# Optimization experiments

Hardware: AMD Instinct MI355X
Metric: run time of the kernel (lower is better)

## Reference

```python
import jax, jax.numpy as jnp
import numpy as np

EMB = 64
D = 2 * EMB          # 128, feature dim of R / hidden of attention MLP
B, L = 128, 4096     # batch, sequence length
N_ITER = 50          # bisection iterations (entmax_bisect default)


def entmax_bisect(X, alpha, n_iter=N_ITER):
    """alpha-entmax via bisection over the last axis. X: [B, L], alpha: [B, 1] (>1)."""
    am1 = alpha - 1.0
    Xs = X * am1
    d = X.shape[-1]
    inv = 1.0 / am1
    max_val = jnp.max(Xs, axis=-1, keepdims=True)
    tau_lo0 = max_val - 1.0                       # gp(1, alpha) = 1
    tau_hi = max_val - (1.0 / d) ** am1           # gp(1/d, alpha)

    def p(tau):
        return jnp.clip(Xs - tau, 0.0, None) ** inv

    f_lo = jnp.sum(p(tau_lo0), axis=-1, keepdims=True) - 1.0

    def body(i, carry):
        tau_lo, dm, _ = carry
        dm = dm * 0.5
        tau_m = tau_lo + dm
        f_m = jnp.sum(p(tau_m), axis=-1, keepdims=True) - 1.0
        tau_lo = jnp.where(f_m * f_lo >= 0, tau_m, tau_lo)
        return (tau_lo, dm, tau_m)

    _, _, tau_m = jax.lax.fori_loop(0, n_iter, body, (tau_lo0, tau_hi - tau_lo0, tau_lo0))
    p_m = p(tau_m)
    return p_m / jnp.sum(p_m, axis=-1, keepdims=True)  # ensure_sum_one


def setup_inputs() -> dict:
    key = jax.random.key(0)
    ks = jax.random.split(key, 9)
    s = 1.0 / np.sqrt(D)
    R = jax.random.normal(ks[0], (B, L, D), dtype=jnp.float32)
    alpha = 1.25 + 0.5 * jax.random.uniform(ks[1], (B, 1), dtype=jnp.float32)  # in (1.25, 1.75)
    target = jax.random.normal(ks[2], (B, 1, D), dtype=jnp.float32)
    Wr1 = s * jax.random.normal(ks[3], (D, D), dtype=jnp.float32)      # Linear(2E, 2E), no bias
    Wr2 = s * jax.random.normal(ks[4], (D, EMB), dtype=jnp.float32)    # Linear(E, 2E) (shape-fixed), no bias
    Wr3 = s * jax.random.normal(ks[5], (1, D), dtype=jnp.float32)      # Linear(2E, 1), no bias
    bias_r = s * jax.random.normal(ks[6], (D,), dtype=jnp.float32)
    Wf_w = s * jax.random.normal(ks[7], (EMB, D), dtype=jnp.float32)   # Linear(2E, E)
    Wf_b = s * jax.random.normal(ks[8], (EMB,), dtype=jnp.float32)
    return {"R": R, "alpha": alpha, "target": target, "Wr1": Wr1, "Wr2": Wr2,
            "Wr3": Wr3, "bias_r": bias_r, "Wf_w": Wf_w, "Wf_b": Wf_b}


def reference(R, alpha, target, Wr1, Wr2, Wr3, bias_r, Wf_w, Wf_b):
    # q = Wf(target): [B, 1, E]
    q = jnp.einsum('btd,ed->bte', target, Wf_w) + Wf_b
    # additive attention score: Wr3 @ relu(Wr1 k + Wr2 q + b): [B, L]
    h = jax.nn.relu(jnp.einsum('bld,ed->ble', R, Wr1)
                    + jnp.einsum('bte,de->btd', q, Wr2)
                    + bias_r)
    scores = jnp.einsum('bld,d->bl', h, Wr3[0])
    # entmax sparsification over the sequence axis
    a = entmax_bisect(scores, alpha)
    # weighted sum of v = R: [B, D]
    res = jnp.einsum('bl,bld->bd', a, R)
    res = jax.nn.selu(res)
    res = res / jnp.linalg.norm(res, axis=-1, keepdims=True)
    return res
```

## Files before the change

kernel.cpp:

```cpp
#include <hip/hip_runtime.h>
#include <hip/hip_bf16.h>

#define B_ 128
#define L_ 4096
#define D_ 128
#define E_ 64

typedef __attribute__((ext_vector_type(8))) short short8;
typedef __attribute__((ext_vector_type(4))) float floatx4;

static __device__ __forceinline__ void split_trunc(float x, unsigned short& hs,
                                                   unsigned short& ls) {
  unsigned int bx = __float_as_uint(x);
  float hf = __uint_as_float(bx & 0xffff0000u);
  hs = (unsigned short)(bx >> 16);
  float lo = x - hf;
  ls = (unsigned short)(__float_as_uint(lo) >> 16);
}

__global__ __launch_bounds__(256) void prep(
    const float* __restrict__ Wr1, unsigned short* __restrict__ hi,
    unsigned short* __restrict__ lo, const float* __restrict__ target,
    const float* __restrict__ Wr2, const float* __restrict__ bias_r,
    const float* __restrict__ Wf_w, const float* __restrict__ Wf_b,
    float* __restrict__ cvec) {
  if (blockIdx.x < 64) {
    int t = blockIdx.x * 256 + threadIdx.x;
    int j = t & 7, lane = (t >> 3) & 63, ks = (t >> 9) & 3, nt = t >> 11;
    int e = nt * 16 + (lane & 15);
    int d = ks * 32 + (lane >> 4) * 8 + j;
    split_trunc(Wr1[e * D_ + d], hi[t], lo[t]);
  } else {
    const int sub = threadIdx.x >> 7;
    const int t = threadIdx.x & 127;
    const int b = (blockIdx.x - 64) * 2 + sub;
    __shared__ float tg[2][D_];
    __shared__ float q[2][E_];
    tg[sub][t] = target[b * D_ + t];
    __syncthreads();
    if (t < E_) {
      float s = Wf_b[t];
      #pragma unroll 8
      for (int d = 0; d < D_; ++d) s += tg[sub][d] * Wf_w[t * D_ + d];
      q[sub][t] = s;
    }
    __syncthreads();
    float s = bias_r[t];
    #pragma unroll 8
    for (int e = 0; e < E_; ++e) s += q[sub][e] * Wr2[t * E_ + e];
    cvec[b * D_ + t] = s;
  }
}

__global__ __launch_bounds__(256, 4) void pass_b(
    const float* __restrict__ R, const unsigned short* __restrict__ Whi,
    const unsigned short* __restrict__ Wlo, const float* __restrict__ cvec,
    const float* __restrict__ Wr3, float* __restrict__ scores) {
  __shared__ __align__(16) unsigned short sAhi[8192];
  __shared__ __align__(16) unsigned short sAlo[8192];
  __shared__ float red[256];

  const int b = blockIdx.x >> 6;
  const int lt = blockIdx.x & 63;
  const int t = threadIdx.x;
  const int wave = t >> 6, lane = t & 63;
  const int col = lane & 15, quad = lane >> 4;

  float w3[2], cb[2];
  #pragma unroll
  for (int n = 0; n < 2; ++n) {
    const int e = (wave * 2 + n) * 16 + col;
    w3[n] = Wr3[e];
    cb[n] = cvec[b * D_ + e];
  }

  const float* Rbase = R + ((size_t)b * L_ + (size_t)lt * 64) * D_;
  #pragma unroll
  for (int ks = 0; ks < 4; ++ks) {
    const int row = wave * 16 + col;
    const int c0 = ks * 32 + quad * 8;
    const float4* p = (const float4*)(Rbase + (size_t)row * D_ + c0);
    float4 v0 = p[0], v1 = p[1];
    float vv[8] = {v0.x, v0.y, v0.z, v0.w, v1.x, v1.y, v1.z, v1.w};
    union { unsigned short u[8]; short8 v; } H, Lo;
    #pragma unroll
    for (int j = 0; j < 8; ++j) split_trunc(vv[j], H.u[j], Lo.u[j]);
    const int base = ((wave * 4 + ks) * 64 + lane) * 8;
    *(short8*)(sAhi + base) = H.v;
    *(short8*)(sAlo + base) = Lo.v;
  }

  short8 bh[2][4], bl[2][4];
  #pragma unroll
  for (int n = 0; n < 2; ++n)
    #pragma unroll
    for (int ks = 0; ks < 4; ++ks) {
      const int off = (((wave * 2 + n) * 4 + ks) * 64 + lane) * 8;
      bh[n][ks] = *(const short8*)(Whi + off);
      bl[n][ks] = *(const short8*)(Wlo + off);
    }

  floatx4 acc[4][2];
  #pragma unroll
  for (int mt = 0; mt < 4; ++mt)
    #pragma unroll
    for (int n = 0; n < 2; ++n) acc[mt][n] = (floatx4){0.f, 0.f, 0.f, 0.f};

  __syncthreads();

  #pragma unroll
  for (int mt = 0; mt < 4; ++mt) {
    #pragma unroll
    for (int ks = 0; ks < 4; ++ks) {
      const int ai = ((mt * 4 + ks) * 64 + lane) * 8;
      short8 ah = *(const short8*)(sAhi + ai);
      short8 al = *(const short8*)(sAlo + ai);
      #pragma unroll
      for (int n = 0; n < 2; ++n) {
        acc[mt][n] = __builtin_amdgcn_mfma_f32_16x16x32_bf16(ah, bh[n][ks], acc[mt][n], 0, 0, 0);
        acc[mt][n] = __builtin_amdgcn_mfma_f32_16x16x32_bf16(al, bh[n][ks], acc[mt][n], 0, 0, 0);
        acc[mt][n] = __builtin_amdgcn_mfma_f32_16x16x32_bf16(ah, bl[n][ks], acc[mt][n], 0, 0, 0);
      }
    }
  }

  float part[4][4];
  #pragma unroll
  for (int mt = 0; mt < 4; ++mt)
    #pragma unroll
    for (int r = 0; r < 4; ++r) {
      float s = 0.f;
      #pragma unroll
      for (int n = 0; n < 2; ++n)
        s += w3[n] * fmaxf(acc[mt][n][r] + cb[n], 0.f);
      s += __shfl_xor(s, 1, 64);
      s += __shfl_xor(s, 2, 64);
      s += __shfl_xor(s, 4, 64);
      s += __shfl_xor(s, 8, 64);
      part[mt][r] = s;
    }
  __syncthreads();
  if (col == 0) {
    #pragma unroll
    for (int mt = 0; mt < 4; ++mt)
      #pragma unroll
      for (int r = 0; r < 4; ++r)
        red[wave * 64 + mt * 16 + quad * 4 + r] = part[mt][r];
  }
  __syncthreads();
  if (t < 64) {
    float s = (red[t] + red[64 + t]) + (red[128 + t] + red[192 + t]);
    scores[(size_t)b * L_ + lt * 64 + t] = s;
  }
}

__global__ __launch_bounds__(512) void pass_cd(
    const float* __restrict__ scores, const float* __restrict__ alpha,
    const float* __restrict__ R, float* __restrict__ out) {
  const int b = blockIdx.x, t = threadIdx.x;
  const int wave = t >> 6, lane = t & 63;
  __shared__ float sred[2][8];
  __shared__ unsigned short sidx[L_];
  __shared__ float sw[L_];
  __shared__ float ppart[512];
  __shared__ int scnt;
  const float am1 = alpha[b] - 1.0f;
  const float inv = 1.0f / am1;
  const float* S = scores + (size_t)b * L_;
  float Xs[8];
  #pragma unroll
  for (int i = 0; i < 8; ++i) Xs[i] = S[i * 512 + t] * am1;
  if (t == 0) scnt = 0;

  float mx = Xs[0];
  #pragma unroll
  for (int i = 1; i < 8; ++i) mx = fmaxf(mx, Xs[i]);
  #pragma unroll
  for (int m = 32; m >= 1; m >>= 1) mx = fmaxf(mx, __shfl_xor(mx, m, 64));
  if (lane == 0) sred[0][wave] = mx;
  __syncthreads();
  mx = sred[0][0];
  #pragma unroll
  for (int w = 1; w < 8; ++w) mx = fmaxf(mx, sred[0][w]);

  float tau_lo = mx - 1.0f;
  float dm = (mx - exp2f(-12.0f * am1)) - tau_lo;

  int pc = 1;
  auto sumP = [&](float tau) -> float {
    const int par = pc & 1;
    ++pc;
    float s = 0.f;
    #pragma unroll
    for (int i = 0; i < 8; ++i) {
      float u = Xs[i] - tau;
      if (u > 0.f) s += exp2f(inv * __log2f(u));
    }
    #pragma unroll
    for (int m = 32; m >= 1; m >>= 1) s += __shfl_xor(s, m, 64);
    if (lane == 0) sred[par][wave] = s;
    __syncthreads();
    float r = sred[par][0];
    #pragma unroll
    for (int w = 1; w < 8; ++w) r += sred[par][w];
    return r;
  };

  const float f_lo = sumP(tau_lo) - 1.0f;
  float tau_m = tau_lo;
  for (int it = 0; it < 24; ++it) {
    dm *= 0.5f;
    tau_m = tau_lo + dm;
    float f_m = sumP(tau_m) - 1.0f;
    if (f_m * f_lo >= 0.f) tau_lo = tau_m;
  }

  float s = 0.f;
  #pragma unroll
  for (int i = 0; i < 8; ++i) {
    float u = Xs[i] - tau_m;
    if (u > 0.f) {
      float p = exp2f(inv * __log2f(u));
      s += p;
      int pos = atomicAdd(&scnt, 1);
      sidx[pos] = (unsigned short)(i * 512 + t);
      sw[pos] = p;
    }
  }
  {
    const int par = pc & 1;
    ++pc;
    #pragma unroll
    for (int m = 32; m >= 1; m >>= 1) s += __shfl_xor(s, m, 64);
    if (lane == 0) sred[par][wave] = s;
    __syncthreads();
    s = sred[par][0];
    #pragma unroll
    for (int w = 1; w < 8; ++w) s += sred[par][w];
  }
  const int ns = scnt;
  const float rs = 1.0f / s;

  const float* Rb = R + (size_t)b * L_ * D_;
  const int g = t >> 7, c = t & 127;
  float acc = 0.f;
  int k = g;
  for (; k + 4 < ns; k += 8) {
    int i0 = sidx[k], i1 = sidx[k + 4];
    float w0 = sw[k], w1 = sw[k + 4];
    acc += w0 * Rb[(size_t)i0 * D_ + c] + w1 * Rb[(size_t)i1 * D_ + c];
  }
  for (; k < ns; k += 4) acc += sw[k] * Rb[(size_t)sidx[k] * D_ + c];
  __syncthreads();
  ppart[t] = acc;
  __syncthreads();
  float r = 0.f;
  if (t < 128) {
    float a2 = ((ppart[t] + ppart[t + 128]) + (ppart[t + 256] + ppart[t + 384])) * rs;
    const float sc = 1.0507009873554805f, al = 1.6732632423543772f;
    r = a2 > 0.f ? sc * a2 : sc * al * (expf(a2) - 1.0f);
  }
  float q = r * r;
  #pragma unroll
  for (int m = 32; m >= 1; m >>= 1) q += __shfl_xor(q, m, 64);
  if (lane == 0) sred[0][wave] = q;
  __syncthreads();
  if (t < 128) {
    float nrm = sqrtf(sred[0][0] + sred[0][1]);
    out[b * D_ + t] = r / nrm;
  }
}

extern "C" void kernel_launch(void* const* d_in, const int* in_sizes, int n_in,
                              void* d_out, int out_size, void* d_ws, size_t ws_size,
                              hipStream_t stream) {
  const float* R      = (const float*)d_in[0];
  const float* alpha  = (const float*)d_in[1];
  const float* target = (const float*)d_in[2];
  const float* Wr1    = (const float*)d_in[3];
  const float* Wr2    = (const float*)d_in[4];
  const float* Wr3    = (const float*)d_in[5];
  const float* bias_r = (const float*)d_in[6];
  const float* Wf_w   = (const float*)d_in[7];
  const float* Wf_b   = (const float*)d_in[8];
  float* out = (float*)d_out;

  char* ws = (char*)d_ws;
  float* cvec          = (float*)ws;
  unsigned short* whi  = (unsigned short*)(ws + 65536);
  unsigned short* wlo  = (unsigned short*)(ws + 98304);
  float* scores        = (float*)(ws + 131072);

  hipLaunchKernelGGL(prep, dim3(128), dim3(256), 0, stream,
                     Wr1, whi, wlo, target, Wr2, bias_r, Wf_w, Wf_b, cvec);
  hipLaunchKernelGGL(pass_b, dim3(B_ * 64), dim3(256), 0, stream,
                     R, whi, wlo, cvec, Wr3, scores);
  hipLaunchKernelGGL(pass_cd, dim3(B_), dim3(512), 0, stream,
                     scores, alpha, R, out);
}
```

Measured before the change: 429.9 us.

## Split sparse weighted gather into separate multi-block kernel with float4 loads

The entmax pass now only writes the compacted support indices and normalized weights to global memory. A new kernel gathers rows of R across 8 blocks per batch, using float4 loads and 4-way unrolling, and a final small kernel reduces the partials and applies SELU and normalization. This raises parallelism for the gather, which previously ran on only 128 blocks, at the cost of two extra launches and global round trips. The score kernel also reorders its MFMA accumulation per tile to lower register pressure and drops a barrier.

```diff
diff --git a/kernel.cpp b/kernel.cpp
--- a/kernel.cpp
+++ b/kernel.cpp
@@ -5,6 +5,7 @@
 #define L_ 4096
 #define D_ 128
 #define E_ 64
+#define GQ 8
 
 typedef __attribute__((ext_vector_type(8))) short short8;
 typedef __attribute__((ext_vector_type(4))) float floatx4;
@@ -100,16 +101,14 @@
       bl[n][ks] = *(const short8*)(Wlo + off);
     }
 
-  floatx4 acc[4][2];
-  #pragma unroll
-  for (int mt = 0; mt < 4; ++mt)
-    #pragma unroll
-    for (int n = 0; n < 2; ++n) acc[mt][n] = (floatx4){0.f, 0.f, 0.f, 0.f};
-
-  __syncthreads();
-
+  __syncthreads();
+
+  float part[4][4];
   #pragma unroll
   for (int mt = 0; mt < 4; ++mt) {
+    floatx4 acc[2];
+    acc[0] = (floatx4){0.f, 0.f, 0.f, 0.f};
+    acc[1] = (floatx4){0.f, 0.f, 0.f, 0.f};
     #pragma unroll
     for (int ks = 0; ks < 4; ++ks) {
       const int ai = ((mt * 4 + ks) * 64 + lane) * 8;
@@ -117,29 +116,25 @@
       short8 al = *(const short8*)(sAlo + ai);
       #pragma unroll
       for (int n = 0; n < 2; ++n) {
-        acc[mt][n] = __builtin_amdgcn_mfma_f32_16x16x32_bf16(ah, bh[n][ks], acc[mt][n], 0, 0, 0);
-        acc[mt][n] = __builtin_amdgcn_mfma_f32_16x16x32_bf16(al, bh[n][ks], acc[mt][n], 0, 0, 0);
-        acc[mt][n] = __builtin_amdgcn_mfma_f32_16x16x32_bf16(ah, bl[n][ks], acc[mt][n], 0, 0, 0);
+        acc[n] = __builtin_amdgcn_mfma_f32_16x16x32_bf16(ah, bh[n][ks], acc[n], 0, 0, 0);
+        acc[n] = __builtin_amdgcn_mfma_f32_16x16x32_bf16(al, bh[n][ks], acc[n], 0, 0, 0);
+        acc[n] = __builtin_amdgcn_mfma_f32_16x16x32_bf16(ah, bl[n][ks], acc[n], 0, 0, 0);
       }
     }
-  }
-
-  float part[4][4];
-  #pragma unroll
-  for (int mt = 0; mt < 4; ++mt)
     #pragma unroll
     for (int r = 0; r < 4; ++r) {
       float s = 0.f;
       #pragma unroll
       for (int n = 0; n < 2; ++n)
-        s += w3[n] * fmaxf(acc[mt][n][r] + cb[n], 0.f);
+        s += w3[n] * fmaxf(acc[n][r] + cb[n], 0.f);
       s += __shfl_xor(s, 1, 64);
       s += __shfl_xor(s, 2, 64);
       s += __shfl_xor(s, 4, 64);
       s += __shfl_xor(s, 8, 64);
       part[mt][r] = s;
     }
-  __syncthreads();
+  }
+
   if (col == 0) {
     #pragma unroll
     for (int mt = 0; mt < 4; ++mt)
@@ -154,15 +149,15 @@
   }
 }
 
-__global__ __launch_bounds__(512) void pass_cd(
+__global__ __launch_bounds__(512) void pass_c(
     const float* __restrict__ scores, const float* __restrict__ alpha,
-    const float* __restrict__ R, float* __restrict__ out) {
+    unsigned short* __restrict__ sidxg, float* __restrict__ swg,
+    int* __restrict__ cntg) {
   const int b = blockIdx.x, t = threadIdx.x;
   const int wave = t >> 6, lane = t & 63;
   __shared__ float sred[2][8];
   __shared__ unsigned short sidx[L_];
   __shared__ float sw[L_];
-  __shared__ float ppart[512];
   __shared__ int scnt;
   const float am1 = alpha[b] - 1.0f;
   const float inv = 1.0f / am1;
@@ -241,34 +236,81 @@
   const int ns = scnt;
   const float rs = 1.0f / s;
 
-  const float* Rb = R + (size_t)b * L_ * D_;
-  const int g = t >> 7, c = t & 127;
-  float acc = 0.f;
-  int k = g;
-  for (; k + 4 < ns; k += 8) {
-    int i0 = sidx[k], i1 = sidx[k + 4];
-    float w0 = sw[k], w1 = sw[k + 4];
-    acc += w0 * Rb[(size_t)i0 * D_ + c] + w1 * Rb[(size_t)i1 * D_ + c];
-  }
-  for (; k < ns; k += 4) acc += sw[k] * Rb[(size_t)sidx[k] * D_ + c];
-  __syncthreads();
-  ppart[t] = acc;
-  __syncthreads();
-  float r = 0.f;
-  if (t < 128) {
-    float a2 = ((ppart[t] + ppart[t + 128]) + (ppart[t + 256] + ppart[t + 384])) * rs;
-    const float sc = 1.0507009873554805f, al = 1.6732632423543772f;
-    r = a2 > 0.f ? sc * a2 : sc * al * (expf(a2) - 1.0f);
-  }
-  float q = r * r;
-  #pragma unroll
-  for (int m = 32; m >= 1; m >>= 1) q += __shfl_xor(q, m, 64);
-  if (lane == 0) sred[0][wave] = q;
-  __syncthreads();
-  if (t < 128) {
-    float nrm = sqrtf(sred[0][0] + sred[0][1]);
-    out[b * D_ + t] = r / nrm;
-  }
+  for (int j = t; j < ns; j += 512) {
+    sidxg[(size_t)b * L_ + j] = sidx[j];
+    swg[(size_t)b * L_ + j] = sw[j] * rs;
+  }
+  if (t == 0) cntg[b] = ns;
+}
+
+__global__ __launch_bounds__(256) void pass_g(
+    const unsigned short* __restrict__ sidxg, const float* __restrict__ swg,
+    const int* __restrict__ cntg, const float* __restrict__ R,
+    float* __restrict__ partial) {
+  const int b = blockIdx.x >> 3, q = blockIdx.x & 7;
+  const int t = threadIdx.x;
+  const int ns = cntg[b];
+  const int per = (ns + GQ - 1) / GQ;
+  const int k0 = q * per;
+  int len = ns - k0;
+  if (len > per) len = per;
+  if (len < 0) len = 0;
+
+  __shared__ unsigned short si[512];
+  __shared__ float swl[512];
+  __shared__ floatx4 red4[8][32];
+
+  for (int j = t; j < len; j += 256) {
+    si[j] = sidxg[(size_t)b * L_ + k0 + j];
+    swl[j] = swg[(size_t)b * L_ + k0 + j];
+  }
+  __syncthreads();
+
+  const int dq = t & 31, sl = t >> 5;
+  const floatx4* R4 = (const floatx4*)(R + (size_t)b * L_ * D_);
+  floatx4 acc = (floatx4){0.f, 0.f, 0.f, 0.f};
+  int j = sl;
+  for (; j + 24 < len; j += 32) {
+    const int i0 = si[j], i1 = si[j + 8], i2 = si[j + 16], i3 = si[j + 24];
+    const float w0 = swl[j], w1 = swl[j + 8], w2 = swl[j + 16], w3 = swl[j + 24];
+    floatx4 r0 = R4[i0 * 32 + dq];
+    floatx4 r1 = R4[i1 * 32 + dq];
+    floatx4 r2 = R4[i2 * 32 + dq];
+    floatx4 r3 = R4[i3 * 32 + dq];
+    acc += w0 * r0;
+    acc += w1 * r1;
+    acc += w2 * r2;
+    acc += w3 * r3;
+  }
+  for (; j < len; j += 8) acc += swl[j] * R4[si[j] * 32 + dq];
+
+  red4[sl][dq] = acc;
+  __syncthreads();
+  if (t < 32) {
+    floatx4 s = red4[0][t];
+    #pragma unroll
+    for (int w = 1; w < 8; ++w) s += red4[w][t];
+    *(floatx4*)(partial + (((size_t)b * GQ + q) * 32 + t) * 4) = s;
+  }
+}
+
+__global__ __launch_bounds__(128) void pass_f(const float* __restrict__ partial,
+                                              float* __restrict__ out) {
+  const int b = blockIdx.x, t = threadIdx.x;
+  const int wave = t >> 6, lane = t & 63;
+  __shared__ float s2[2];
+  float v = 0.f;
+  #pragma unroll
+  for (int q = 0; q < GQ; ++q) v += partial[((size_t)b * GQ + q) * D_ + t];
+  const float sc = 1.0507009873554805f, al = 1.6732632423543772f;
+  float r = v > 0.f ? sc * v : sc * al * (expf(v) - 1.0f);
+  float qq = r * r;
+  #pragma unroll
+  for (int m = 32; m >= 1; m >>= 1) qq += __shfl_xor(qq, m, 64);
+  if (lane == 0) s2[wave] = qq;
+  __syncthreads();
+  const float nrm = sqrtf(s2[0] + s2[1]);
+  out[(size_t)b * D_ + t] = r / nrm;
 }
 
 extern "C" void kernel_launch(void* const* d_in, const int* in_sizes, int n_in,
@@ -290,11 +332,19 @@
   unsigned short* whi  = (unsigned short*)(ws + 65536);
   unsigned short* wlo  = (unsigned short*)(ws + 98304);
   float* scores        = (float*)(ws + 131072);
+  unsigned short* sidxg= (unsigned short*)(ws + 2228224);
+  float* swg           = (float*)(ws + 3276800);
+  int* cntg            = (int*)(ws + 5373952);
+  float* partial       = (float*)(ws + 5374464);
 
   hipLaunchKernelGGL(prep, dim3(128), dim3(256), 0, stream,
                      Wr1, whi, wlo, target, Wr2, bias_r, Wf_w, Wf_b, cvec);
   hipLaunchKernelGGL(pass_b, dim3(B_ * 64), dim3(256), 0, stream,
                      R, whi, wlo, cvec, Wr3, scores);
-  hipLaunchKernelGGL(pass_cd, dim3(B_), dim3(512), 0, stream,
-                     scores, alpha, R, out);
-}
+  hipLaunchKernelGGL(pass_c, dim3(B_), dim3(512), 0, stream,
+                     scores, alpha, sidxg, swg, cntg);
+  hipLaunchKernelGGL(pass_g, dim3(B_ * GQ), dim3(256), 0, stream,
+                     sidxg, swg, cntg, R, partial);
+  hipLaunchKernelGGL(pass_f, dim3(B_), dim3(128), 0, stream,
+                     partial, out);
+}
```

After: 403.4 us, median of 2. -6.2%, faster.
